# Performance work log

Hardware: AMD Instinct MI355X
Metric: run time of the kernel (lower is better)

## Reference

```python
import jax, jax.numpy as jnp
import numpy as np

N_CLASS, N_SUPPORT, N_QUERY = 5, 5, 15
C, T, V = 128, 8, 25
LN_EPS = 1e-12


def setup_inputs() -> dict:
    key = jax.random.key(0)
    ks = jax.random.split(key, 6)
    n_tot = N_CLASS * (N_SUPPORT + N_QUERY)
    inp = jax.random.normal(ks[0], (n_tot, C, T, V), dtype=jnp.float32)
    # episode labels: 20 consecutive samples per class (arange // per_class)
    target = (jnp.arange(n_tot, dtype=jnp.int32) // (N_SUPPORT + N_QUERY)).astype(jnp.int32)
    s = 0.02
    p = lambda k: jax.random.normal(k, (C, C), dtype=jnp.float32) * s
    return {
        'input': inp,
        'Wq': p(ks[1]), 'bq': jnp.zeros((C,), jnp.float32),
        'Wk': p(ks[2]), 'bk': jnp.zeros((C,), jnp.float32),
        'Wv': p(ks[3]), 'bv': jnp.zeros((C,), jnp.float32),
        'Wo': p(ks[4]), 'bo': jnp.zeros((C,), jnp.float32),
        'ln_g': jnp.ones((C,), jnp.float32), 'ln_b': jnp.zeros((C,), jnp.float32),
        'target': target,
        'n_support': N_SUPPORT,
    }


def _layer_norm(x, g, b):
    mu = x.mean(-1, keepdims=True)
    var = ((x - mu) ** 2).mean(-1, keepdims=True)
    return (x - mu) * jax.lax.rsqrt(var + LN_EPS) * g + b


def _episode_forward(input, Wq, bq, Wk, bk, Wv, bv, Wo, bo, ln_g, ln_b, target, n_support):
    n_tot, c, t, v = input.shape
    m = N_CLASS
    per_class = n_tot // m
    n_query = per_class - n_support
    n = m * n_query

    # support/query split (stable argsort == torch.where per class for sorted labels)
    order = jnp.argsort(target).reshape(m, per_class)
    supp_idx = order[:, :n_support]                      # (m, h)
    qry_idx = order[:, n_support:].reshape(-1)           # (n,)
    z_proto = input[supp_idx]                            # (m, h, c, t, v)
    zq = input[qry_idx]                                  # (n, c, t, v)

    # ---- hal(): pairwise cross-attention over the vertex axis ----
    mh = m * n_support
    zq_p = jnp.transpose(zq, (0, 2, 3, 1))                                   # (n, t, v, c)
    zp_p = jnp.transpose(z_proto.reshape(mh, c, t, v), (0, 2, 3, 1))          # (mh, t, v, c)
    cat = jnp.concatenate([zq_p, zp_p], axis=0)                               # (n1, t, v, c)
    n1 = cat.shape[0]

    # Q from each of the n1 items, K/V from each of the mh prototypes.
    # Equivalent to the original expand->reshape pairing, without duplicating K/V.
    Q = cat @ Wq + bq                                                         # (n1, t, v, c)
    K = zp_p @ Wk + bk                                                        # (mh, t, v, c)
    Vv = zp_p @ Wv + bv                                                       # (mh, t, v, c)
    scale = 1.0 / jnp.sqrt(jnp.asarray(c, dtype=Q.dtype))
    scores = jnp.einsum('ntqc,mtkc->nmtqk', Q, K) * scale                     # (n1, mh, t, v, v)
    attn = jax.nn.softmax(scores, axis=-1)
    ctx = jnp.einsum('nmtqk,mtkc->nmtqc', attn, Vv)                           # (n1, mh, t, v, c)
    out = _layer_norm(ctx @ Wo + bo + cat[:, None], ln_g, ln_b)               # residual + LN
    att = out.mean(axis=1)                                                    # (n1, t, v, c) mean over mh pairs

    zq_att = jnp.transpose(att[:n], (0, 3, 1, 2))                             # (n, c, t, v)
    proto_att = att[n:].reshape(m, n_support, t, v, c).mean(axis=1)           # (m, t, v, c)
    proto_att = jnp.transpose(proto_att, (0, 3, 1, 2))                        # (m, c, t, v)

    # ---- squared-Euclidean metric on flattened features ----
    zq_f = zq_att.reshape(n, -1)
    zp_f = proto_att.reshape(m, -1)
    dist = jnp.sum((zq_f[:, None, :] - zp_f[None, :, :]) ** 2, axis=-1)       # (n, m)

    log_p_y = jax.nn.log_softmax(-dist, axis=1).reshape(m, n_query, m)
    cls = jnp.arange(m)
    loss = -log_p_y[cls[:, None], jnp.arange(n_query)[None, :], cls[:, None]].mean()
    y_hat = jnp.argmax(log_p_y, axis=2)
    acc = (y_hat == cls[:, None]).astype(jnp.float32).mean()
    return loss, acc


def reference(input, Wq, bq, Wk, bk, Wv, bv, Wo, bo, ln_g, ln_b, target, n_support):
    return _episode_forward(input, Wq, bq, Wk, bk, Wv, bv, Wo, bo, ln_g, ln_b, target, n_support)
```

## Files before the change

### kernel.cpp

```cpp
#include <hip/hip_runtime.h>
#include <math.h>

#define NTOT 100
#define NQ   75
#define NP   25
#define CC   128
#define TT   8
#define VV   25
#define NCLS 5
#define NSUP 5
#define NQRY 15
#define ROW  (TT*VV*CC)
#define TILE (VV*CC)
#define ROWS_Q 20000
#define ROWS_S 5000
#define RB_Q 625
#define RB_S 157

typedef __attribute__((ext_vector_type(8))) short short8;
typedef __attribute__((ext_vector_type(16))) float f32x16;

__device__ __forceinline__ ushort f2bf(float f) {
    uint u = __float_as_uint(f);
    u += 0x7FFFu + ((u >> 16) & 1u);
    return (ushort)(u >> 16);
}
__device__ __forceinline__ float bf2f(uint u16v) {
    return __uint_as_float(u16v << 16);
}

__global__ __launch_bounds__(256) void k_prep(
    const float* __restrict__ input, const int* __restrict__ target,
    const float* __restrict__ Wq, const float* __restrict__ Wk,
    const float* __restrict__ Wv, const float* __restrict__ Wo,
    ushort* __restrict__ catQbf, ushort* __restrict__ catSbf,
    ushort* __restrict__ Wfrag, ushort* __restrict__ catC,
    float* __restrict__ proto, int* __restrict__ counter) {
    __shared__ float smp[100 * 129];
    __shared__ int targ[NTOT];
    __shared__ int order[NTOT];
    int b = blockIdx.x, tid = threadIdx.x;

    if (b < 200) {
        int n = b >> 1, hf = b & 1;
        if (tid < NTOT) targ[tid] = target[tid];
        __syncthreads();
        if (tid < NTOT) {
            int ti = targ[tid], rank = 0;
            for (int j = 0; j < NTOT; ++j) {
                int tj = targ[j];
                rank += (tj < ti) || (tj == ti && j < tid);
            }
            order[rank] = tid;
        }
        __syncthreads();
        int src;
        if (n < NQ) { int m = n / NQRY, qq = n - m * NQRY; src = order[m * 20 + NSUP + qq]; }
        else        { int i = n - NQ; int m = i / NSUP, s = i - m * NSUP; src = order[m * 20 + s]; }

        const float* in = input + (size_t)src * ROW + hf * 100;
        for (int idx = tid; idx < 12800; idx += 256) {
            int c = idx / 100, tt = idx - c * 100;
            smp[tt * 129 + c] = in[c * 200 + tt];
        }
        __syncthreads();
        uint* cc = (uint*)catC + ((size_t)n * 200 + hf * 100) * 64;
        for (int e2 = tid; e2 < 6400; e2 += 256) {
            int r = e2 >> 6, c2 = e2 & 63;
            float f0 = smp[r * 129 + c2 * 2], f1 = smp[r * 129 + c2 * 2 + 1];
            cc[r * 64 + c2] = (uint)f2bf(f0) | ((uint)f2bf(f1) << 16);
        }
        bool isSup = (n >= NQ);
        for (int o = tid; o < 1600; o += 256) {
            int k8 = o / 100, tt = o - k8 * 100;
            int base = tt * 129 + k8 * 8;
            uint4 pk;
            pk.x = (uint)f2bf(smp[base+0]) | ((uint)f2bf(smp[base+1]) << 16);
            pk.y = (uint)f2bf(smp[base+2]) | ((uint)f2bf(smp[base+3]) << 16);
            pk.z = (uint)f2bf(smp[base+4]) | ((uint)f2bf(smp[base+5]) << 16);
            pk.w = (uint)f2bf(smp[base+6]) | ((uint)f2bf(smp[base+7]) << 16);
            int row = n * 200 + hf * 100 + tt;
            size_t dst = (((size_t)(row >> 5) * 8 + (k8 >> 1)) * 64 + ((row & 31) + 32 * (k8 & 1))) * 8;
            *(uint4*)(catQbf + dst) = pk;
            if (isSup) {
                int r2 = (n - NQ) * 200 + hf * 100 + tt;
                size_t dst2 = (((size_t)(r2 >> 5) * 8 + (k8 >> 1)) * 64 + ((r2 & 31) + 32 * (k8 & 1))) * 8;
                *(uint4*)(catSbf + dst2) = pk;
            }
        }
    } else if (b < 204) {
        int wi = b - 200;
        const float* W = (wi == 0) ? Wq : (wi == 1) ? Wk : (wi == 2) ? Wv : Wo;
        ushort* dstW = Wfrag + (size_t)wi * 16384;
        for (int o = tid; o < 2048; o += 256) {
            int k8 = o >> 7, c = o & 127;
            uint4 pk;
            float f0 = W[(k8*8+0)*128 + c], f1 = W[(k8*8+1)*128 + c];
            float f2 = W[(k8*8+2)*128 + c], f3 = W[(k8*8+3)*128 + c];
            float f4 = W[(k8*8+4)*128 + c], f5 = W[(k8*8+5)*128 + c];
            float f6 = W[(k8*8+6)*128 + c], f7 = W[(k8*8+7)*128 + c];
            pk.x = (uint)f2bf(f0) | ((uint)f2bf(f1) << 16);
            pk.y = (uint)f2bf(f2) | ((uint)f2bf(f3) << 16);
            pk.z = (uint)f2bf(f4) | ((uint)f2bf(f5) << 16);
            pk.w = (uint)f2bf(f6) | ((uint)f2bf(f7) << 16);
            size_t dst = ((size_t)((c >> 5) * 8 + (k8 >> 1)) * 64 + ((c & 31) + 32 * (k8 & 1))) * 8;
            *(uint4*)(dstW + dst) = pk;
        }
        if (wi == 3) {
            uint4 z = make_uint4(0, 0, 0, 0);
            for (int o = tid; o < 512; o += 256) {
                int ks = o >> 6, l = o & 63;
                if ((l & 31) >= 8)
                    *(uint4*)(catSbf + (((size_t)156 * 8 + ks) * 64 + l) * 8) = z;
            }
        }
    } else {
        for (int i = tid; i < NCLS * ROW; i += 256) proto[i] = 0.f;
        if (tid == 0) *counter = 0;
    }
}

__global__ __launch_bounds__(256) void k_proj(
    const ushort* __restrict__ catQbf, const ushort* __restrict__ catSbf,
    const ushort* __restrict__ Wfrag, const float* __restrict__ bq,
    const float* __restrict__ bk, const float* __restrict__ bv,
    ushort* __restrict__ Qf, ushort* __restrict__ Kf, ushort* __restrict__ Vf) {
    __shared__ ushort Vt[128 * 136];
    int b = blockIdx.x, tid = threadIdx.x;
    int w = tid >> 6, lane = tid & 63;
    int typ, rb0, nrb;
    if (b < 157)      { typ = 0; rb0 = b * 4;         nrb = RB_Q; }
    else if (b < 197) { typ = 1; rb0 = (b - 157) * 4; nrb = RB_S; }
    else              { typ = 2; rb0 = (b - 197) * 4; nrb = RB_S; }
    int rowblk = rb0 + w;
    bool act = rowblk < nrb;
    const ushort* src = (typ == 0) ? catQbf : catSbf;
    const ushort* Wf = Wfrag + (size_t)typ * 16384;
    const float* bias = (typ == 0) ? bq : (typ == 1) ? bk : bv;
    int rlimit = (typ == 0) ? ROWS_Q : ROWS_S;

    short8 af[8];
    if (act) {
        const ushort* ap = src + (size_t)rowblk * 4096 + lane * 8;
        #pragma unroll
        for (int ks = 0; ks < 8; ++ks) af[ks] = *(const short8*)(ap + ks * 512);
    }
    #pragma unroll
    for (int ct = 0; ct < 4; ++ct) {
        f32x16 Cm;
        #pragma unroll
        for (int r = 0; r < 16; ++r) Cm[r] = 0.f;
        if (act) {
            const ushort* bp = Wf + (size_t)(ct * 8) * 512 + lane * 8;
            #pragma unroll
            for (int ks = 0; ks < 8; ++ks) {
                short8 bf_ = *(const short8*)(bp + ks * 512);
                Cm = __builtin_amdgcn_mfma_f32_32x32x16_bf16(af[ks], bf_, Cm, 0, 0, 0);
            }
            float bcol = bias[ct * 32 + (lane & 31)];
            if (typ <= 1) {
                ushort* dstB = (typ == 0) ? Qf : Kf;
                #pragma unroll
                for (int r = 0; r < 16; ++r) {
                    int row = rowblk * 32 + (r & 3) + 8 * (r >> 2) + 4 * (lane >> 5);
                    if (row < rlimit) {
                        int c = ct * 32 + (lane & 31);
                        int st = row / 25, vv = row - st * 25;
                        size_t dst = (((size_t)st * 8 + (c >> 4)) * 64 + (vv + 32 * ((c >> 3) & 1))) * 8 + (c & 7);
                        dstB[dst] = f2bf(Cm[r] + bcol);
                    }
                }
            } else {
                #pragma unroll
                for (int r = 0; r < 16; ++r) {
                    int lrow = w * 32 + (r & 3) + 8 * (r >> 2) + 4 * (lane >> 5);
                    Vt[lrow * 136 + ct * 32 + (lane & 31)] = f2bf(Cm[r] + bcol);
                }
            }
        }
    }
    if (typ == 2) {
        __syncthreads();
        const ushort* WoF = Wfrag + (size_t)3 * 16384;
        short8 a2[8];
        if (act) {
            #pragma unroll
            for (int ks = 0; ks < 8; ++ks)
                a2[ks] = *(const short8*)(Vt + (w * 32 + (lane & 31)) * 136 + ks * 16 + (lane >> 5) * 8);
        }
        #pragma unroll
        for (int ct = 0; ct < 4; ++ct) {
            if (act) {
                f32x16 Cm;
                #pragma unroll
                for (int r = 0; r < 16; ++r) Cm[r] = 0.f;
                const ushort* bp = WoF + (size_t)(ct * 8) * 512 + lane * 8;
                #pragma unroll
                for (int ks = 0; ks < 8; ++ks) {
                    short8 bf_ = *(const short8*)(bp + ks * 512);
                    Cm = __builtin_amdgcn_mfma_f32_32x32x16_bf16(a2[ks], bf_, Cm, 0, 0, 0);
                }
                #pragma unroll
                for (int r = 0; r < 16; ++r) {
                    int row = rowblk * 32 + (r & 3) + 8 * (r >> 2) + 4 * (lane >> 5);
                    if (row < ROWS_S) {
                        int c = ct * 32 + (lane & 31);
                        int tile = row / 25, vv = row - tile * 25;
                        size_t dst = ((((size_t)tile * 4 + ct) * 2 + (vv >> 4)) * 64
                                      + ((c & 31) + 32 * ((vv & 15) >> 3))) * 8 + (vv & 7);
                        Vf[dst] = f2bf(Cm[r]);
                    }
                }
            }
        }
    }
}

__global__ __launch_bounds__(256, 2) void k_attn(
    const ushort* __restrict__ Qf, const ushort* __restrict__ Kf,
    const ushort* __restrict__ Vf, const ushort* __restrict__ catC,
    const float* __restrict__ bo, float* __restrict__ att,
    float* __restrict__ proto) {
    __shared__ float catb[25 * 129];
    __shared__ float red[2][50][65];
    __shared__ ushort qls[4096];
    ushort* pfragU = (ushort*)red;

    int pair = blockIdx.x;
    int n = pair >> 3, t = pair & 7;
    int tid = threadIdx.x;
    int wv = tid >> 6, lane = tid & 63;
    int q = lane & 31, half = lane >> 5;

    {
        const uint* cc = (const uint*)catC + (size_t)pair * 1600;
        for (int i2 = tid; i2 < 1600; i2 += 256) {
            uint u = cc[i2];
            int r = i2 >> 6, c2 = (i2 & 63) * 2;
            catb[r * 129 + c2]     = bf2f(u & 0xffffu) + bo[c2];
            catb[r * 129 + c2 + 1] = bf2f(u >> 16) + bo[c2 + 1];
        }
    }
    {
        const uint* qp = (const uint*)(Qf + (size_t)pair * 4096);
        uint* ql = (uint*)qls;
        for (int i2 = tid; i2 < 2048; i2 += 256) ql[i2] = qp[i2];
    }
    {
        uint4 z = make_uint4(0, 0, 0, 0);
        *(uint4*)&pfragU[(((wv * 2 + 0) * 64) + lane) * 8] = z;
        *(uint4*)&pfragU[(((wv * 2 + 1) * 64) + lane) * 8] = z;
    }
    __syncthreads();

    int qc = q < 25 ? q : 24;
    float attsum[64];
    #pragma unroll
    for (int i = 0; i < 64; ++i) attsum[i] = 0.f;
    float Csc = 0.f;

    const float CEXP = (float)(1.4426950408889634 * 0.08838834764831845);

    const ushort* kbase = Kf + (size_t)t * 4096 + lane * 8;
    short8 kf[8];
    #pragma unroll
    for (int ks = 0; ks < 8; ++ks)
        kf[ks] = *(const short8*)(kbase + (size_t)wv * 32768 + ks * 512);

    for (int m = wv; m < 25; m += 4) {
        f32x16 S;
        #pragma unroll
        for (int r = 0; r < 16; ++r) S[r] = 0.f;
        #pragma unroll
        for (int ks = 0; ks < 8; ++ks) {
            short8 qv = *(const short8*)(qls + ks * 512 + lane * 8);
            S = __builtin_amdgcn_mfma_f32_32x32x16_bf16(kf[ks], qv, S, 0, 0, 0);
        }

        float p[16], mx = -3e38f;
        #pragma unroll
        for (int r = 0; r < 16; ++r) {
            int key = (r & 3) + 8 * (r >> 2) + 4 * half;
            float v = (key < 25) ? S[r] : -3e38f;
            p[r] = v; mx = fmaxf(mx, v);
        }
        mx = fmaxf(mx, __shfl_xor(mx, 32));
        float sum = 0.f;
        #pragma unroll
        for (int r = 0; r < 16; ++r) { p[r] = exp2f((p[r] - mx) * CEXP); sum += p[r]; }
        sum += __shfl_xor(sum, 32);
        float inv = 1.f / sum;

        const ushort* vp = Vf + ((size_t)(m * 8 + t)) * 4096 + lane * 8;
        short8 vf0 = *(const short8*)(vp);
        short8 vf1 = *(const short8*)(vp + 512);
        short8 vf2 = *(const short8*)(vp + 1024);
        short8 vf3 = *(const short8*)(vp + 1536);
        short8 vf4 = *(const short8*)(vp + 2048);
        short8 vf5 = *(const short8*)(vp + 2560);
        short8 vf6 = *(const short8*)(vp + 3072);
        short8 vf7 = *(const short8*)(vp + 3584);

        #pragma unroll
        for (int r = 0; r < 16; ++r) {
            int key = (r & 3) + 8 * (r >> 2) + 4 * half;
            if (key < 25)
                pfragU[(((wv * 2 + (key >> 4)) * 64) + (q + 32 * ((key >> 3) & 1))) * 8 + (key & 7)]
                    = f2bf(p[r] * inv);
        }
        short8 pb0 = *(const short8*)&pfragU[(((wv * 2 + 0) * 64) + lane) * 8];
        short8 pb1 = *(const short8*)&pfragU[(((wv * 2 + 1) * 64) + lane) * 8];

        f32x16 ctx[4];
        #pragma unroll
        for (int mt = 0; mt < 4; ++mt) {
            #pragma unroll
            for (int r = 0; r < 16; ++r) ctx[mt][r] = 0.f;
        }
        ctx[0] = __builtin_amdgcn_mfma_f32_32x32x16_bf16(vf0, pb0, ctx[0], 0, 0, 0);
        ctx[0] = __builtin_amdgcn_mfma_f32_32x32x16_bf16(vf1, pb1, ctx[0], 0, 0, 0);
        ctx[1] = __builtin_amdgcn_mfma_f32_32x32x16_bf16(vf2, pb0, ctx[1], 0, 0, 0);
        ctx[1] = __builtin_amdgcn_mfma_f32_32x32x16_bf16(vf3, pb1, ctx[1], 0, 0, 0);
        ctx[2] = __builtin_amdgcn_mfma_f32_32x32x16_bf16(vf4, pb0, ctx[2], 0, 0, 0);
        ctx[2] = __builtin_amdgcn_mfma_f32_32x32x16_bf16(vf5, pb1, ctx[2], 0, 0, 0);
        ctx[3] = __builtin_amdgcn_mfma_f32_32x32x16_bf16(vf6, pb0, ctx[3], 0, 0, 0);
        ctx[3] = __builtin_amdgcn_mfma_f32_32x32x16_bf16(vf7, pb1, ctx[3], 0, 0, 0);

        short8 kfn[8];
        #pragma unroll
        for (int ks = 0; ks < 8; ++ks)
            kfn[ks] = *(const short8*)(kbase + (size_t)(m + 4) * 32768 + ks * 512);

        float s1 = 0.f, s2 = 0.f;
        #pragma unroll
        for (int mt = 0; mt < 4; ++mt) {
            #pragma unroll
            for (int r = 0; r < 16; ++r) {
                int c = mt * 32 + (r & 3) + 8 * (r >> 2) + 4 * half;
                float xv = ctx[mt][r] + catb[qc * 129 + c];
                ctx[mt][r] = xv;
                s1 += xv; s2 = fmaf(xv, xv, s2);
            }
        }
        s1 += __shfl_xor(s1, 32); s2 += __shfl_xor(s2, 32);
        float mu = s1 * (1.f / 128.f);
        float var = s2 * (1.f / 128.f) - mu * mu;
        var = fmaxf(var, 0.f);
        float rs = rsqrtf(var + 1e-12f);
        #pragma unroll
        for (int i = 0; i < 64; ++i)
            attsum[i] = fmaf(ctx[i >> 4][i & 15], rs, attsum[i]);
        Csc = fmaf(-mu, rs, Csc);

        #pragma unroll
        for (int ks = 0; ks < 8; ++ks) kf[ks] = kfn[ks];
    }

    __syncthreads();
    int s = half * 25 + q;
    bool act = q < 25;
    if ((wv == 1 || wv == 3) && act) {
        float (*rg)[65] = red[wv >> 1];
        #pragma unroll
        for (int i = 0; i < 64; ++i) rg[s][i] = attsum[i];
        rg[s][64] = Csc;
    }
    __syncthreads();
    if ((wv == 0 || wv == 2) && act) {
        float (*rg)[65] = red[wv >> 1];
        #pragma unroll
        for (int i = 0; i < 64; ++i) attsum[i] += rg[s][i];
        Csc += rg[s][64];
    }
    __syncthreads();
    if (wv == 2 && act) {
        #pragma unroll
        for (int i = 0; i < 64; ++i) red[0][s][i] = attsum[i];
        red[0][s][64] = Csc;
    }
    __syncthreads();
    if (wv == 0 && act) {
        #pragma unroll
        for (int i = 0; i < 64; ++i) attsum[i] += red[0][s][i];
        Csc += red[0][s][64];
        if (n < NQ) {
            float* ap = att + (size_t)pair * TILE + q * 128;
            #pragma unroll
            for (int mt = 0; mt < 4; ++mt) {
                #pragma unroll
                for (int rg4 = 0; rg4 < 4; ++rg4) {
                    int c0 = mt * 32 + 8 * rg4 + 4 * half;
                    int i0 = mt * 16 + rg4 * 4;
                    float4 o;
                    o.x = attsum[i0 + 0] + Csc; o.y = attsum[i0 + 1] + Csc;
                    o.z = attsum[i0 + 2] + Csc; o.w = attsum[i0 + 3] + Csc;
                    *(float4*)&ap[c0] = o;
                }
            }
        } else {
            int cls = (n - NQ) / NSUP;
            float* pp = proto + (size_t)cls * ROW + t * TILE + q * 128;
            #pragma unroll
            for (int mt = 0; mt < 4; ++mt) {
                #pragma unroll
                for (int r = 0; r < 16; ++r) {
                    int c = mt * 32 + (r & 3) + 8 * (r >> 2) + 4 * half;
                    atomicAdd(&pp[c], (attsum[mt * 16 + r] + Csc) * 0.2f);
                }
            }
        }
    }
}

__global__ __launch_bounds__(256) void k_dist_loss(
    const float* __restrict__ att, const float* __restrict__ proto,
    const float* __restrict__ ln_g, float* __restrict__ dist,
    int* __restrict__ counter, float* __restrict__ out) {
    int b = blockIdx.x;
    int i = b / 5, j = b - 5 * i;
    const float4* a = (const float4*)(att + (size_t)i * ROW);
    const float4* p = (const float4*)(proto + (size_t)j * ROW);
    float d = 0.f;
    for (int e4 = threadIdx.x; e4 < 6400; e4 += 256) {
        float4 av = a[e4], pv = p[e4];
        float4 g4 = *(const float4*)(ln_g + (e4 & 31) * 4);
        float dx = av.x - pv.x, dy = av.y - pv.y;
        float dz = av.z - pv.z, dw = av.w - pv.w;
        d = fmaf(g4.x * g4.x, dx * dx, d);
        d = fmaf(g4.y * g4.y, dy * dy, d);
        d = fmaf(g4.z * g4.z, dz * dz, d);
        d = fmaf(g4.w * g4.w, dw * dw, d);
    }
    #pragma unroll
    for (int msk = 32; msk >= 1; msk >>= 1) d += __shfl_xor(d, msk);
    __shared__ float part[4];
    __shared__ int lastFlag;
    int lane = threadIdx.x & 63, wv = threadIdx.x >> 6;
    if (lane == 0) part[wv] = d;
    __syncthreads();
    if (threadIdx.x == 0) {
        float total = (part[0] + part[1] + part[2] + part[3]) * (1.f / 625.f);
        __hip_atomic_store(&dist[b], total, __ATOMIC_RELEASE, __HIP_MEMORY_SCOPE_AGENT);
        int tk = __hip_atomic_fetch_add(counter, 1, __ATOMIC_ACQ_REL, __HIP_MEMORY_SCOPE_AGENT);
        lastFlag = (tk == 374);
    }
    __syncthreads();
    if (!lastFlag) return;

    int iq = threadIdx.x;
    float li = 0.f, ok = 0.f;
    if (iq < NQ) {
        float dd[5];
        #pragma unroll
        for (int jj = 0; jj < 5; ++jj)
            dd[jj] = __hip_atomic_load(&dist[iq * 5 + jj], __ATOMIC_ACQUIRE, __HIP_MEMORY_SCOPE_AGENT);
        int cls = iq / NQRY;
        float mind = dd[0];
        int best = 0;
        #pragma unroll
        for (int jj = 1; jj < 5; ++jj) {
            if (dd[jj] < mind) mind = dd[jj];
            if (dd[jj] < dd[best]) best = jj;
        }
        float sume = 0.f;
        #pragma unroll
        for (int jj = 0; jj < 5; ++jj) sume += expf(mind - dd[jj]);
        float lse = logf(sume) - mind;
        li = dd[cls] + lse;
        ok = (best == cls) ? 1.f : 0.f;
    }
    #pragma unroll
    for (int msk = 32; msk >= 1; msk >>= 1) {
        li += __shfl_xor(li, msk);
        ok += __shfl_xor(ok, msk);
    }
    if (lane == 0) { part[wv] = li; part[wv + 2] = ok; }
    __syncthreads();
    if (threadIdx.x == 0) {
        out[0] = (part[0] + part[1]) / 75.f;
        out[1] = (part[2] + part[3]) / 75.f;
    }
}

extern "C" void kernel_launch(void* const* d_in, const int* in_sizes, int n_in,
                              void* d_out, int out_size, void* d_ws, size_t ws_size,
                              hipStream_t stream) {
    const float* input = (const float*)d_in[0];
    const float* Wq   = (const float*)d_in[1];
    const float* bq   = (const float*)d_in[2];
    const float* Wk   = (const float*)d_in[3];
    const float* bk   = (const float*)d_in[4];
    const float* Wv   = (const float*)d_in[5];
    const float* bv   = (const float*)d_in[6];
    const float* Wo   = (const float*)d_in[7];
    const float* bo   = (const float*)d_in[8];
    const float* ln_g = (const float*)d_in[9];
    const float* ln_b = (const float*)d_in[10];
    const int* target = (const int*)d_in[11];
    float* out = (float*)d_out;
    (void)ln_b;

    float* ws = (float*)d_ws;
    ushort* catQbf = (ushort*)ws;
    ushort* catSbf = catQbf + (size_t)RB_Q * 4096;
    ushort* Wfrag  = catSbf + (size_t)RB_S * 4096;
    ushort* catC   = Wfrag + 65536;
    ushort* Qf     = catC + 2560000;
    ushort* Kf     = Qf + 3276800;
    ushort* Vf     = Kf + 819200;
    float*  att    = (float*)(Vf + 819200);
    float*  proto  = att + 1920000;
    float*  distb  = proto + 128000;
    int*    counter= (int*)(distb + 512);

    k_prep<<<205, 256, 0, stream>>>(input, target, Wq, Wk, Wv, Wo,
                                    catQbf, catSbf, Wfrag, catC, proto, counter);
    k_proj<<<237, 256, 0, stream>>>(catQbf, catSbf, Wfrag, bq, bk, bv, Qf, Kf, Vf);
    k_attn<<<800, 256, 0, stream>>>(Qf, Kf, Vf, catC, bo, att, proto);
    k_dist_loss<<<375, 256, 0, stream>>>(att, proto, ln_g, distb, counter, out);
}
```

Baseline: 187.3 us.

## Pipeline next QK score MFMA in attention loop and drop prototype atomics

The attention loop now computes the next prototype's QK^T scores right after the softmax of the current one, so MFMA work overlaps the LayerNorm/epilogue, and it prefetches K two steps ahead. Support items now write their full attention output to the att buffer instead of atomically accumulating into a zeroed proto buffer, and the distance kernel averages the five support rows on the fly. This removes the proto zeroing block and the float atomics, in exchange for five extra row reads per distance block and more live registers in the attention kernel.

```diff
diff --git a/kernel.cpp b/kernel.cpp
--- a/kernel.cpp
+++ b/kernel.cpp
@@ -35,7 +35,7 @@
     const float* __restrict__ Wv, const float* __restrict__ Wo,
     ushort* __restrict__ catQbf, ushort* __restrict__ catSbf,
     ushort* __restrict__ Wfrag, ushort* __restrict__ catC,
-    float* __restrict__ proto, int* __restrict__ counter) {
+    int* __restrict__ counter) {
     __shared__ float smp[100 * 129];
     __shared__ int targ[NTOT];
     __shared__ int order[NTOT];
@@ -88,7 +88,7 @@
                 *(uint4*)(catSbf + dst2) = pk;
             }
         }
-    } else if (b < 204) {
+    } else {
         int wi = b - 200;
         const float* W = (wi == 0) ? Wq : (wi == 1) ? Wk : (wi == 2) ? Wv : Wo;
         ushort* dstW = Wfrag + (size_t)wi * 16384;
@@ -113,10 +113,8 @@
                 if ((l & 31) >= 8)
                     *(uint4*)(catSbf + (((size_t)156 * 8 + ks) * 64 + l) * 8) = z;
             }
-        }
-    } else {
-        for (int i = tid; i < NCLS * ROW; i += 256) proto[i] = 0.f;
-        if (tid == 0) *counter = 0;
+            if (tid == 0) *counter = 0;
+        }
     }
 }
 
@@ -219,15 +217,14 @@
 __global__ __launch_bounds__(256, 2) void k_attn(
     const ushort* __restrict__ Qf, const ushort* __restrict__ Kf,
     const ushort* __restrict__ Vf, const ushort* __restrict__ catC,
-    const float* __restrict__ bo, float* __restrict__ att,
-    float* __restrict__ proto) {
+    const float* __restrict__ bo, float* __restrict__ att) {
     __shared__ float catb[25 * 129];
     __shared__ float red[2][50][65];
     __shared__ ushort qls[4096];
     ushort* pfragU = (ushort*)red;
 
     int pair = blockIdx.x;
-    int n = pair >> 3, t = pair & 7;
+    int t = pair & 7;
     int tid = threadIdx.x;
     int wv = tid >> 6, lane = tid & 63;
     int q = lane & 31, half = lane >> 5;
@@ -262,20 +259,26 @@
     const float CEXP = (float)(1.4426950408889634 * 0.08838834764831845);
 
     const ushort* kbase = Kf + (size_t)t * 4096 + lane * 8;
-    short8 kf[8];
+    short8 kb[8];
     #pragma unroll
     for (int ks = 0; ks < 8; ++ks)
-        kf[ks] = *(const short8*)(kbase + (size_t)wv * 32768 + ks * 512);
-
-    for (int m = wv; m < 25; m += 4) {
-        f32x16 S;
-        #pragma unroll
-        for (int r = 0; r < 16; ++r) S[r] = 0.f;
-        #pragma unroll
-        for (int ks = 0; ks < 8; ++ks) {
-            short8 qv = *(const short8*)(qls + ks * 512 + lane * 8);
-            S = __builtin_amdgcn_mfma_f32_32x32x16_bf16(kf[ks], qv, S, 0, 0, 0);
-        }
+        kb[ks] = *(const short8*)(kbase + (size_t)wv * 32768 + ks * 512);
+
+    f32x16 S;
+    #pragma unroll
+    for (int r = 0; r < 16; ++r) S[r] = 0.f;
+    #pragma unroll
+    for (int ks = 0; ks < 8; ++ks) {
+        short8 qv = *(const short8*)(qls + ks * 512 + lane * 8);
+        S = __builtin_amdgcn_mfma_f32_32x32x16_bf16(kb[ks], qv, S, 0, 0, 0);
+    }
+    #pragma unroll
+    for (int ks = 0; ks < 8; ++ks)
+        kb[ks] = *(const short8*)(kbase + (size_t)(wv + 4) * 32768 + ks * 512);
+
+    int cnt = (wv == 0) ? 7 : 6;
+    for (int mi = 0; mi < cnt; ++mi) {
+        int m = wv + 4 * mi;
 
         float p[16], mx = -3e38f;
         #pragma unroll
@@ -308,6 +311,19 @@
                 pfragU[(((wv * 2 + (key >> 4)) * 64) + (q + 32 * ((key >> 3) & 1))) * 8 + (key & 7)]
                     = f2bf(p[r] * inv);
         }
+
+        f32x16 Sn;
+        #pragma unroll
+        for (int r = 0; r < 16; ++r) Sn[r] = 0.f;
+        #pragma unroll
+        for (int ks = 0; ks < 8; ++ks) {
+            short8 qv = *(const short8*)(qls + ks * 512 + lane * 8);
+            Sn = __builtin_amdgcn_mfma_f32_32x32x16_bf16(kb[ks], qv, Sn, 0, 0, 0);
+        }
+        #pragma unroll
+        for (int ks = 0; ks < 8; ++ks)
+            kb[ks] = *(const short8*)(kbase + (size_t)(m + 8) * 32768 + ks * 512);
+
         short8 pb0 = *(const short8*)&pfragU[(((wv * 2 + 0) * 64) + lane) * 8];
         short8 pb1 = *(const short8*)&pfragU[(((wv * 2 + 1) * 64) + lane) * 8];
 
@@ -326,21 +342,18 @@
         ctx[3] = __builtin_amdgcn_mfma_f32_32x32x16_bf16(vf6, pb0, ctx[3], 0, 0, 0);
         ctx[3] = __builtin_amdgcn_mfma_f32_32x32x16_bf16(vf7, pb1, ctx[3], 0, 0, 0);
 
-        short8 kfn[8];
-        #pragma unroll
-        for (int ks = 0; ks < 8; ++ks)
-            kfn[ks] = *(const short8*)(kbase + (size_t)(m + 4) * 32768 + ks * 512);
-
         float s1 = 0.f, s2 = 0.f;
         #pragma unroll
         for (int mt = 0; mt < 4; ++mt) {
+            float t1 = 0.f, t2 = 0.f;
             #pragma unroll
             for (int r = 0; r < 16; ++r) {
                 int c = mt * 32 + (r & 3) + 8 * (r >> 2) + 4 * half;
                 float xv = ctx[mt][r] + catb[qc * 129 + c];
                 ctx[mt][r] = xv;
-                s1 += xv; s2 = fmaf(xv, xv, s2);
-            }
+                t1 += xv; t2 = fmaf(xv, xv, t2);
+            }
+            s1 += t1; s2 += t2;
         }
         s1 += __shfl_xor(s1, 32); s2 += __shfl_xor(s2, 32);
         float mu = s1 * (1.f / 128.f);
@@ -352,8 +365,7 @@
             attsum[i] = fmaf(ctx[i >> 4][i & 15], rs, attsum[i]);
         Csc = fmaf(-mu, rs, Csc);
 
-        #pragma unroll
-        for (int ks = 0; ks < 8; ++ks) kf[ks] = kfn[ks];
+        S = Sn;
     }
 
     __syncthreads();
@@ -383,49 +395,44 @@
         #pragma unroll
         for (int i = 0; i < 64; ++i) attsum[i] += red[0][s][i];
         Csc += red[0][s][64];
-        if (n < NQ) {
-            float* ap = att + (size_t)pair * TILE + q * 128;
+        float* ap = att + (size_t)pair * TILE + q * 128;
+        #pragma unroll
+        for (int mt = 0; mt < 4; ++mt) {
             #pragma unroll
-            for (int mt = 0; mt < 4; ++mt) {
-                #pragma unroll
-                for (int rg4 = 0; rg4 < 4; ++rg4) {
-                    int c0 = mt * 32 + 8 * rg4 + 4 * half;
-                    int i0 = mt * 16 + rg4 * 4;
-                    float4 o;
-                    o.x = attsum[i0 + 0] + Csc; o.y = attsum[i0 + 1] + Csc;
-                    o.z = attsum[i0 + 2] + Csc; o.w = attsum[i0 + 3] + Csc;
-                    *(float4*)&ap[c0] = o;
-                }
-            }
-        } else {
-            int cls = (n - NQ) / NSUP;
-            float* pp = proto + (size_t)cls * ROW + t * TILE + q * 128;
-            #pragma unroll
-            for (int mt = 0; mt < 4; ++mt) {
-                #pragma unroll
-                for (int r = 0; r < 16; ++r) {
-                    int c = mt * 32 + (r & 3) + 8 * (r >> 2) + 4 * half;
-                    atomicAdd(&pp[c], (attsum[mt * 16 + r] + Csc) * 0.2f);
-                }
+            for (int rg4 = 0; rg4 < 4; ++rg4) {
+                int c0 = mt * 32 + 8 * rg4 + 4 * half;
+                int i0 = mt * 16 + rg4 * 4;
+                float4 o;
+                o.x = attsum[i0 + 0] + Csc; o.y = attsum[i0 + 1] + Csc;
+                o.z = attsum[i0 + 2] + Csc; o.w = attsum[i0 + 3] + Csc;
+                *(float4*)&ap[c0] = o;
             }
         }
     }
 }
 
 __global__ __launch_bounds__(256) void k_dist_loss(
-    const float* __restrict__ att, const float* __restrict__ proto,
-    const float* __restrict__ ln_g, float* __restrict__ dist,
-    int* __restrict__ counter, float* __restrict__ out) {
+    const float* __restrict__ att, const float* __restrict__ ln_g,
+    float* __restrict__ dist, int* __restrict__ counter,
+    float* __restrict__ out) {
     int b = blockIdx.x;
     int i = b / 5, j = b - 5 * i;
-    const float4* a = (const float4*)(att + (size_t)i * ROW);
-    const float4* p = (const float4*)(proto + (size_t)j * ROW);
+    const float4* a  = (const float4*)(att + (size_t)i * ROW);
+    const float4* s0 = (const float4*)(att + (size_t)(NQ + j * 5 + 0) * ROW);
+    const float4* s1p = (const float4*)(att + (size_t)(NQ + j * 5 + 1) * ROW);
+    const float4* s2p = (const float4*)(att + (size_t)(NQ + j * 5 + 2) * ROW);
+    const float4* s3p = (const float4*)(att + (size_t)(NQ + j * 5 + 3) * ROW);
+    const float4* s4p = (const float4*)(att + (size_t)(NQ + j * 5 + 4) * ROW);
     float d = 0.f;
     for (int e4 = threadIdx.x; e4 < 6400; e4 += 256) {
-        float4 av = a[e4], pv = p[e4];
+        float4 av = a[e4];
+        float4 q0 = s0[e4], q1 = s1p[e4], q2 = s2p[e4], q3 = s3p[e4], q4 = s4p[e4];
         float4 g4 = *(const float4*)(ln_g + (e4 & 31) * 4);
-        float dx = av.x - pv.x, dy = av.y - pv.y;
-        float dz = av.z - pv.z, dw = av.w - pv.w;
+        float px = 0.2f * (q0.x + q1.x + q2.x + q3.x + q4.x);
+        float py = 0.2f * (q0.y + q1.y + q2.y + q3.y + q4.y);
+        float pz = 0.2f * (q0.z + q1.z + q2.z + q3.z + q4.z);
+        float pw = 0.2f * (q0.w + q1.w + q2.w + q3.w + q4.w);
+        float dx = av.x - px, dy = av.y - py, dz = av.z - pz, dw = av.w - pw;
         d = fmaf(g4.x * g4.x, dx * dx, d);
         d = fmaf(g4.y * g4.y, dy * dy, d);
         d = fmaf(g4.z * g4.z, dz * dz, d);
@@ -509,13 +516,12 @@
     ushort* Kf     = Qf + 3276800;
     ushort* Vf     = Kf + 819200;
     float*  att    = (float*)(Vf + 819200);
-    float*  proto  = att + 1920000;
-    float*  distb  = proto + 128000;
+    float*  distb  = att + 2560000;
     int*    counter= (int*)(distb + 512);
 
-    k_prep<<<205, 256, 0, stream>>>(input, target, Wq, Wk, Wv, Wo,
-                                    catQbf, catSbf, Wfrag, catC, proto, counter);
+    k_prep<<<204, 256, 0, stream>>>(input, target, Wq, Wk, Wv, Wo,
+                                    catQbf, catSbf, Wfrag, catC, counter);
     k_proj<<<237, 256, 0, stream>>>(catQbf, catSbf, Wfrag, bq, bk, bv, Qf, Kf, Vf);
-    k_attn<<<800, 256, 0, stream>>>(Qf, Kf, Vf, catC, bo, att, proto);
-    k_dist_loss<<<375, 256, 0, stream>>>(att, proto, ln_g, distb, counter, out);
-}
+    k_attn<<<800, 256, 0, stream>>>(Qf, Kf, Vf, catC, bo, att);
+    k_dist_loss<<<375, 256, 0, stream>>>(att, ln_g, distb, counter, out);
+}
```

Measured after the change: 203.8 us. 8.8% more time.
